# Kernel tuning notes

Measured on AMD Instinct MI355X. Metric: run time of the kernel, lower is better.

The kernel has to match this reference:

```python
import jax, jax.numpy as jnp
import numpy as np

N, T, D, H = 256, 256, 1024, 1024


def setup_inputs() -> dict:
    key = jax.random.key(0)
    k1, k2, k3, k4, k5, k6 = jax.random.split(key, 6)
    encoded_subjects = jax.random.normal(k1, (N, T, D), dtype=jnp.float32)
    encoded_objects = jax.random.normal(k2, (N, T, D), dtype=jnp.float32)
    # pair_ffn: Linear(2D -> H), ReLU, Linear(H -> 1); torch Linear stores W as [out, in]
    lim1 = 1.0 / np.sqrt(2 * D)
    W1 = jax.random.uniform(k3, (H, 2 * D), dtype=jnp.float32, minval=-lim1, maxval=lim1)
    b1 = jax.random.uniform(k4, (H,), dtype=jnp.float32, minval=-lim1, maxval=lim1)
    lim2 = 1.0 / np.sqrt(H)
    W2 = jax.random.uniform(k5, (1, H), dtype=jnp.float32, minval=-lim2, maxval=lim2)
    b2 = jax.random.uniform(k6, (1,), dtype=jnp.float32, minval=-lim2, maxval=lim2)
    return {
        "encoded_subjects": encoded_subjects,
        "encoded_objects": encoded_objects,
        "W1": W1,
        "b1": b1,
        "W2": W2,
        "b2": b2,
    }


def reference(encoded_subjects, encoded_objects, W1, b1, W2, b2):
    # max-pool over token dim -> [N, D]
    sub = jnp.max(encoded_subjects, axis=1)
    obj = jnp.max(encoded_objects, axis=1)
    n = obj.shape[0]
    # cat([sub_i, obj_j]) @ W1.T == sub_i @ W1[:, :D].T + obj_j @ W1[:, D:].T
    d = sub.shape[-1]
    s_part = jnp.einsum("nd,hd->nh", sub, W1[:, :d])  # [N, H]
    o_part = jnp.einsum("nd,hd->nh", obj, W1[:, d:])  # [N, H]
    h = jax.nn.relu(s_part[:, None, :] + o_part[None, :, :] + b1)  # [N, N, H]
    scores = jnp.einsum("ijh,h->ij", h, W2[0]) + b2[0]  # [N, N]
    # diagonal entries stay zero (loop skips i == j)
    pair_matrix = jnp.where(jnp.eye(n, dtype=bool), 0.0, scores)
    return pair_matrix
```

## Files before the change

kernel.cpp:

```cpp
#include <hip/hip_runtime.h>
#include <math.h>

#define NN 256
#define TT 256
#define DD 1024
#define HH 1024

typedef float f32x4 __attribute__((ext_vector_type(4)));
typedef short bf16x8 __attribute__((ext_vector_type(8)));

__device__ inline unsigned short f2bf_rne(float x) {
    unsigned u = __float_as_uint(x);
    unsigned r = (u + 0x7fffu + ((u >> 16) & 1u)) >> 16;
    return (unsigned short)r;
}
__device__ inline float bf2f(unsigned short h) {
    return __uint_as_float(((unsigned)h) << 16);
}

__global__ __launch_bounds__(256) void pool_kernel(const float* __restrict__ subs,
                                                   const float* __restrict__ objs,
                                                   float* __restrict__ pooled) {
    const int n = blockIdx.x;
    const int which = blockIdx.y;
    const f32x4* src = reinterpret_cast<const f32x4*>(which == 0 ? subs : objs);
    const int d4 = threadIdx.x;
    const f32x4* base = src + (((size_t)n) << 16) + d4;

    f32x4 a[8];
#pragma unroll
    for (int s = 0; s < 8; ++s) a[s] = (f32x4){-INFINITY, -INFINITY, -INFINITY, -INFINITY};

    for (int k = 0; k < 256; k += 8) {
        f32x4 v[8];
#pragma unroll
        for (int s = 0; s < 8; ++s)
            v[s] = __builtin_nontemporal_load(base + (size_t)(k + s) * 256);
#pragma unroll
        for (int s = 0; s < 8; ++s) {
#pragma unroll
            for (int e = 0; e < 4; ++e) a[s][e] = fmaxf(a[s][e], v[s][e]);
        }
    }
#pragma unroll
    for (int s = 0; s < 4; ++s)
#pragma unroll
        for (int e = 0; e < 4; ++e) a[s][e] = fmaxf(a[s][e], a[s + 4][e]);
    f32x4 m;
#pragma unroll
    for (int e = 0; e < 4; ++e)
        m[e] = fmaxf(fmaxf(a[0][e], a[1][e]), fmaxf(a[2][e], a[3][e]));

    reinterpret_cast<f32x4*>(pooled)[((size_t)(which * NN + n)) * 256 + d4] = m;
}

__global__ __launch_bounds__(256, 1) void gemm_kernel(const float* __restrict__ A,
                                                      const float* __restrict__ W1,
                                                      const float* __restrict__ b1,
                                                      float* __restrict__ out) {
    __shared__ unsigned short Ah[64 * 40];
    __shared__ unsigned short Al[64 * 40];
    __shared__ unsigned short Bh[32 * 40];
    __shared__ unsigned short Bl[32 * 40];

    const int t = threadIdx.x;
    const int lane = t & 63;
    const int w = t >> 6;
    const int wm = w >> 1, wn = w & 1;
    const int n0 = blockIdx.x * 32;
    const int m0 = blockIdx.y * 64;
    const bool is_sub = (m0 < NN);
    const int koff = is_sub ? 0 : DD;

    const int ar = t >> 2;
    const int akq = (t & 3) * 8;
    const int br = (t & 127) >> 2;
    const int bkq = akq;

    f32x4 acc0 = {0.f, 0.f, 0.f, 0.f};
    f32x4 acc1 = {0.f, 0.f, 0.f, 0.f};

    const int iA0 = (wm * 32 + (lane & 15)) * 40 + (lane >> 4) * 8;
    const int iA1 = (wm * 32 + 16 + (lane & 15)) * 40 + (lane >> 4) * 8;
    const int iB  = (wn * 16 + (lane & 15)) * 40 + (lane >> 4) * 8;

    for (int ch = 0; ch < 32; ++ch) {
        const int kb = ch * 32;
        const float* ap = A + (size_t)(m0 + ar) * DD + kb + akq;
        f32x4 av0 = *(const f32x4*)ap;
        f32x4 av1 = *(const f32x4*)(ap + 4);
        f32x4 bv0, bv1;
        if (t < 128) {
            const float* bp = W1 + (size_t)(n0 + br) * (2 * DD) + koff + kb + bkq;
            bv0 = *(const f32x4*)bp;
            bv1 = *(const f32x4*)(bp + 4);
        }
        __syncthreads();

        {
            float xs[8];
#pragma unroll
            for (int e = 0; e < 4; ++e) { xs[e] = av0[e]; xs[4 + e] = av1[e]; }
            unsigned hw[4], lw[4];
#pragma unroll
            for (int p = 0; p < 4; ++p) {
                unsigned short h0 = f2bf_rne(xs[2 * p]);
                unsigned short h1 = f2bf_rne(xs[2 * p + 1]);
                unsigned short l0 = f2bf_rne(xs[2 * p] - bf2f(h0));
                unsigned short l1 = f2bf_rne(xs[2 * p + 1] - bf2f(h1));
                hw[p] = (unsigned)h0 | ((unsigned)h1 << 16);
                lw[p] = (unsigned)l0 | ((unsigned)l1 << 16);
            }
            *(uint4*)&Ah[ar * 40 + akq] = make_uint4(hw[0], hw[1], hw[2], hw[3]);
            *(uint4*)&Al[ar * 40 + akq] = make_uint4(lw[0], lw[1], lw[2], lw[3]);
        }
        if (t < 128) {
            float xs[8];
#pragma unroll
            for (int e = 0; e < 4; ++e) { xs[e] = bv0[e]; xs[4 + e] = bv1[e]; }
            unsigned hw[4], lw[4];
#pragma unroll
            for (int p = 0; p < 4; ++p) {
                unsigned short h0 = f2bf_rne(xs[2 * p]);
                unsigned short h1 = f2bf_rne(xs[2 * p + 1]);
                unsigned short l0 = f2bf_rne(xs[2 * p] - bf2f(h0));
                unsigned short l1 = f2bf_rne(xs[2 * p + 1] - bf2f(h1));
                hw[p] = (unsigned)h0 | ((unsigned)h1 << 16);
                lw[p] = (unsigned)l0 | ((unsigned)l1 << 16);
            }
            *(uint4*)&Bh[br * 40 + bkq] = make_uint4(hw[0], hw[1], hw[2], hw[3]);
            *(uint4*)&Bl[br * 40 + bkq] = make_uint4(lw[0], lw[1], lw[2], lw[3]);
        }
        __syncthreads();

        bf16x8 a0h = *(const bf16x8*)&Ah[iA0];
        bf16x8 a0l = *(const bf16x8*)&Al[iA0];
        bf16x8 a1h = *(const bf16x8*)&Ah[iA1];
        bf16x8 a1l = *(const bf16x8*)&Al[iA1];
        bf16x8 bh  = *(const bf16x8*)&Bh[iB];
        bf16x8 bl  = *(const bf16x8*)&Bl[iB];

        acc0 = __builtin_amdgcn_mfma_f32_16x16x32_bf16(a0h, bh, acc0, 0, 0, 0);
        acc0 = __builtin_amdgcn_mfma_f32_16x16x32_bf16(a0h, bl, acc0, 0, 0, 0);
        acc0 = __builtin_amdgcn_mfma_f32_16x16x32_bf16(a0l, bh, acc0, 0, 0, 0);
        acc1 = __builtin_amdgcn_mfma_f32_16x16x32_bf16(a1h, bh, acc1, 0, 0, 0);
        acc1 = __builtin_amdgcn_mfma_f32_16x16x32_bf16(a1h, bl, acc1, 0, 0, 0);
        acc1 = __builtin_amdgcn_mfma_f32_16x16x32_bf16(a1l, bh, acc1, 0, 0, 0);
    }

    const int col = n0 + wn * 16 + (lane & 15);
    const float bias = is_sub ? b1[col] : 0.f;
    const int rb = m0 + wm * 32 + (lane >> 4) * 4;
#pragma unroll
    for (int r = 0; r < 4; ++r) {
        out[(size_t)(rb + r) * HH + col] = acc0[r] + bias;
        out[(size_t)(rb + 16 + r) * HH + col] = acc1[r] + bias;
    }
}

#define HC 128

__global__ __launch_bounds__(256) void pair_kernel(const float* __restrict__ sp_op,
                                                   const float* __restrict__ W2,
                                                   const float* __restrict__ b2,
                                                   float* __restrict__ out) {
    __shared__ float oT[16][HC + 4];
    const int t = threadIdx.x;
    const int tx = t & 15, ty = t >> 4;
    const int i0 = blockIdx.y * 16, j0 = blockIdx.x * 16;
    const float* sp = sp_op;
    const float* op = sp_op + (size_t)NN * HH;
    const float* srow = sp + (size_t)(i0 + ty) * HH;

    const int s_row = t >> 5;
    const int s_h = (t & 31) * 4;

    float4 ro[2];
#pragma unroll
    for (int r = 0; r < 2; ++r) {
        const int row = s_row + r * 8;
        ro[r] = *(const float4*)&op[(size_t)(j0 + row) * HH + s_h];
    }

    float acc = 0.f;
    for (int c = 0; c < HH / HC; ++c) {
#pragma unroll
        for (int r = 0; r < 2; ++r) {
            const int row = s_row + r * 8;
            *(float4*)&oT[row][s_h] = ro[r];
        }
        float4 no[2];
        if (c + 1 < HH / HC) {
#pragma unroll
            for (int r = 0; r < 2; ++r) {
                const int row = s_row + r * 8;
                no[r] = *(const float4*)&op[(size_t)(j0 + row) * HH + (c + 1) * HC + s_h];
            }
        }
        __syncthreads();
#pragma unroll
        for (int h4 = 0; h4 < HC / 4; ++h4) {
            float4 s = *(const float4*)&srow[c * HC + h4 * 4];
            float4 o = *(const float4*)&oT[tx][h4 * 4];
            float4 w = *(const float4*)&W2[c * HC + h4 * 4];
            acc += fmaxf(s.x + o.x, 0.f) * w.x;
            acc += fmaxf(s.y + o.y, 0.f) * w.y;
            acc += fmaxf(s.z + o.z, 0.f) * w.z;
            acc += fmaxf(s.w + o.w, 0.f) * w.w;
        }
        __syncthreads();
        if (c + 1 < HH / HC) {
#pragma unroll
            for (int r = 0; r < 2; ++r) { ro[r] = no[r]; }
        }
    }
    const int i = i0 + ty, j = j0 + tx;
    const float score = acc + b2[0];
    out[i * NN + j] = (i == j) ? 0.f : score;
}

extern "C" void kernel_launch(void* const* d_in, const int* in_sizes, int n_in,
                              void* d_out, int out_size, void* d_ws, size_t ws_size,
                              hipStream_t stream) {
    const float* subs = (const float*)d_in[0];
    const float* objs = (const float*)d_in[1];
    const float* W1   = (const float*)d_in[2];
    const float* b1   = (const float*)d_in[3];
    const float* W2   = (const float*)d_in[4];
    const float* b2   = (const float*)d_in[5];
    float* out = (float*)d_out;

    float* pooled = (float*)d_ws;
    float* sp_op  = pooled + (size_t)2 * NN * DD;

    pool_kernel<<<dim3(NN, 2), 256, 0, stream>>>(subs, objs, pooled);
    gemm_kernel<<<dim3(HH / 32, (2 * NN) / 64), 256, 0, stream>>>(pooled, W1, b1, sp_op);
    pair_kernel<<<dim3(NN / 16, NN / 16), 256, 0, stream>>>(sp_op, W2, b2, out);
}
```

Measured before the change: 155.5 us.

## Stage subject rows in swizzled LDS and stream object rows through registers

The pair kernel now loads the block's 16 subject rows in full (64 KB) into shared memory with an XOR swizzle. Each thread streams its own object row from global memory into registers with double buffering, replacing the chunked LDS staging of object rows and the per-chunk barriers. This removes repeated global reads of subject rows and most synchronisation. In exchange it needs 64 KB of LDS and many registers per thread (launch bounds set to one block), which lowers occupancy. The object-row global loads are also no longer coalesced, since each lane reads a different row.

After: 147.7 us. -5.1%, faster.

```diff
diff --git a/kernel.cpp b/kernel.cpp
--- a/kernel.cpp
+++ b/kernel.cpp
@@ -158,60 +158,57 @@
     }
 }
 
-#define HC 128
-
-__global__ __launch_bounds__(256) void pair_kernel(const float* __restrict__ sp_op,
-                                                   const float* __restrict__ W2,
-                                                   const float* __restrict__ b2,
-                                                   float* __restrict__ out) {
-    __shared__ float oT[16][HC + 4];
+__global__ __launch_bounds__(256, 1) void pair_kernel(const float* __restrict__ sp_op,
+                                                      const float* __restrict__ W2,
+                                                      const float* __restrict__ b2,
+                                                      float* __restrict__ out) {
+    __shared__ f32x4 sT4[16 * 256];
     const int t = threadIdx.x;
     const int tx = t & 15, ty = t >> 4;
     const int i0 = blockIdx.y * 16, j0 = blockIdx.x * 16;
     const float* sp = sp_op;
     const float* op = sp_op + (size_t)NN * HH;
-    const float* srow = sp + (size_t)(i0 + ty) * HH;
-
-    const int s_row = t >> 5;
-    const int s_h = (t & 31) * 4;
-
-    float4 ro[2];
-#pragma unroll
-    for (int r = 0; r < 2; ++r) {
-        const int row = s_row + r * 8;
-        ro[r] = *(const float4*)&op[(size_t)(j0 + row) * HH + s_h];
-    }
+
+    {
+        const int srow = t >> 4;
+        const float* sg = sp + (size_t)(i0 + srow) * HH;
+#pragma unroll
+        for (int q = 0; q < 16; ++q) {
+            const int col4 = (t & 15) + 16 * q;
+            sT4[srow * 256 + (col4 ^ (srow & 7))] = *(const f32x4*)&sg[col4 * 4];
+        }
+    }
+
+    const float* orow = op + (size_t)(j0 + tx) * HH;
+    const f32x4* w2v = reinterpret_cast<const f32x4*>(W2);
+
+    f32x4 og[16], ng[16];
+#pragma unroll
+    for (int q = 0; q < 16; ++q) og[q] = *(const f32x4*)&orow[q * 4];
+
+    __syncthreads();
 
     float acc = 0.f;
-    for (int c = 0; c < HH / HC; ++c) {
-#pragma unroll
-        for (int r = 0; r < 2; ++r) {
-            const int row = s_row + r * 8;
-            *(float4*)&oT[row][s_h] = ro[r];
-        }
-        float4 no[2];
-        if (c + 1 < HH / HC) {
-#pragma unroll
-            for (int r = 0; r < 2; ++r) {
-                const int row = s_row + r * 8;
-                no[r] = *(const float4*)&op[(size_t)(j0 + row) * HH + (c + 1) * HC + s_h];
-            }
-        }
-        __syncthreads();
-#pragma unroll
-        for (int h4 = 0; h4 < HC / 4; ++h4) {
-            float4 s = *(const float4*)&srow[c * HC + h4 * 4];
-            float4 o = *(const float4*)&oT[tx][h4 * 4];
-            float4 w = *(const float4*)&W2[c * HC + h4 * 4];
-            acc += fmaxf(s.x + o.x, 0.f) * w.x;
-            acc += fmaxf(s.y + o.y, 0.f) * w.y;
-            acc += fmaxf(s.z + o.z, 0.f) * w.z;
-            acc += fmaxf(s.w + o.w, 0.f) * w.w;
-        }
-        __syncthreads();
-        if (c + 1 < HH / HC) {
-#pragma unroll
-            for (int r = 0; r < 2; ++r) { ro[r] = no[r]; }
+    for (int half = 0; half < 16; ++half) {
+        if (half < 15) {
+            const int nb = (half + 1) * 64;
+#pragma unroll
+            for (int q = 0; q < 16; ++q) ng[q] = *(const f32x4*)&orow[nb + q * 4];
+        }
+#pragma unroll
+        for (int h4 = 0; h4 < 16; ++h4) {
+            const int col4 = half * 16 + h4;
+            f32x4 s = sT4[ty * 256 + (col4 ^ (ty & 7))];
+            f32x4 w = w2v[col4];
+            f32x4 o = og[h4];
+            acc += fmaxf(s[0] + o[0], 0.f) * w[0];
+            acc += fmaxf(s[1] + o[1], 0.f) * w[1];
+            acc += fmaxf(s[2] + o[2], 0.f) * w[2];
+            acc += fmaxf(s[3] + o[3], 0.f) * w[3];
+        }
+        if (half < 15) {
+#pragma unroll
+            for (int q = 0; q < 16; ++q) og[q] = ng[q];
         }
     }
     const int i = i0 + ty, j = j0 + tx;
```
